# Performance work log

Measured on AMD Instinct MI355X. Metric: run time of the kernel, lower is better.

The kernel has to match this reference:

```python
import jax, jax.numpy as jnp
import numpy as np

N_NODES = 100000
N_EDGES = 3200000
FEAT = 16


def gcn_conv(x, src, dst, W, b):
    # PyG GCNConv: add self-loops, symmetric normalization deg^{-1/2}(A+I)deg^{-1/2},
    # then linear transform and scatter-add aggregation.
    n = x.shape[0]
    loop = jnp.arange(n, dtype=src.dtype)
    s = jnp.concatenate([src, loop])
    d = jnp.concatenate([dst, loop])
    deg = jax.ops.segment_sum(jnp.ones_like(d, dtype=x.dtype), d, num_segments=n)
    dinv = jnp.where(deg > 0, jax.lax.rsqrt(deg), 0.0)
    norm = dinv[s] * dinv[d]  # [E+N]
    h = x @ W  # [N, out]
    msg = h[s] * norm[:, None]  # gather + weight
    out = jax.ops.segment_sum(msg, d, num_segments=n)  # scatter-add
    return out + b


def setup_inputs() -> dict:
    key = jax.random.key(0)
    k1, k2, k3, k4 = jax.random.split(key, 4)
    scale = 1.0 / np.sqrt(FEAT)
    return {
        "x": jax.random.normal(k1, (N_NODES, FEAT), dtype=jnp.float32),
        "edge_index": jax.random.randint(k2, (2, N_EDGES), 0, N_NODES, dtype=jnp.int64) if jax.config.jax_enable_x64 else jax.random.randint(k2, (2, N_EDGES), 0, N_NODES, dtype=jnp.int32),
        "W1": jax.random.normal(k3, (FEAT, 16), dtype=jnp.float32) * scale,
        "b1": jnp.zeros((16,), dtype=jnp.float32),
        "W2": jax.random.normal(k4, (16, FEAT), dtype=jnp.float32) * scale,
        "b2": jnp.zeros((FEAT,), dtype=jnp.float32),
    }


def reference(x, edge_index, W1, b1, W2, b2):
    src, dst = edge_index[0], edge_index[1]
    h = gcn_conv(x, src, dst, W1, b1)
    h = jax.nn.relu(h)
    out = gcn_conv(h, src, dst, W2, b2)
    return out
```

## Files before the change

kernel.cpp:

```cpp
#include <hip/hip_runtime.h>

#define F 16
#define BSHIFT 8
#define NPB 256
#define NB 391
#define CH 4096


__global__ void hist_kernel(const int* __restrict__ dst, unsigned* __restrict__ bcount, int E) {
    __shared__ unsigned lc[NB];
    for (int i = threadIdx.x; i < NB; i += blockDim.x) lc[i] = 0;
    __syncthreads();
    int E4 = E >> 2;
    const int4* d4 = (const int4*)dst;
    int stride = gridDim.x * blockDim.x;
    for (int e = blockIdx.x * blockDim.x + threadIdx.x; e < E4; e += stride) {
        int4 v = d4[e];
        atomicAdd(&lc[((unsigned)v.x) >> BSHIFT], 1u);
        atomicAdd(&lc[((unsigned)v.y) >> BSHIFT], 1u);
        atomicAdd(&lc[((unsigned)v.z) >> BSHIFT], 1u);
        atomicAdd(&lc[((unsigned)v.w) >> BSHIFT], 1u);
    }
    for (int e = E4 * 4 + blockIdx.x * blockDim.x + threadIdx.x; e < E; e += stride)
        atomicAdd(&lc[((unsigned)dst[e]) >> BSHIFT], 1u);
    __syncthreads();
    for (int i = threadIdx.x; i < NB; i += blockDim.x) {
        unsigned c = lc[i];
        if (c) atomicAdd(&bcount[i], c);
    }
}

__global__ void scan_kernel(const unsigned* __restrict__ bcount, int* __restrict__ off,
                            unsigned* __restrict__ cursor, int E) {
    __shared__ unsigned s[2048];
    int t = threadIdx.x;
    unsigned c0 = (t < NB) ? bcount[t] : 0u;
    unsigned c1 = (t + 1024 < NB) ? bcount[t + 1024] : 0u;
    s[t] = c0; s[t + 1024] = c1;
    __syncthreads();
    for (int d = 1; d < 2048; d <<= 1) {
        unsigned a  = (t >= d) ? s[t - d] : 0u;
        unsigned bv = (t + 1024 >= d) ? s[t + 1024 - d] : 0u;
        __syncthreads();
        s[t] += a; s[t + 1024] += bv;
        __syncthreads();
    }
    if (t < NB)       { unsigned ex = s[t] - c0;       off[t] = ex;       cursor[t * 16] = ex; }
    if (t + 1024 < NB){ unsigned ex = s[t+1024] - c1;  off[t+1024] = ex;  cursor[(t+1024)*16] = ex; }
    if (t == 0) off[NB] = E;
}

__global__ void reorder_kernel(const int* __restrict__ src, const int* __restrict__ dst,
                               unsigned* __restrict__ cursor, unsigned* __restrict__ recs, int E) {
    __shared__ unsigned lsorted[CH];
    __shared__ unsigned short lbkt[CH];
    __shared__ unsigned lstart[NB + 1];
    __shared__ unsigned lcur[NB];
    __shared__ int ldelta[NB];
    int t = threadIdx.x, b = blockIdx.x;
    int e0 = b * CH;
    int cnt_e = E - e0; if (cnt_e > CH) cnt_e = CH;
    int i4 = cnt_e >> 2;
    const int4* dst4 = (const int4*)(dst + e0);
    const int4* src4 = (const int4*)(src + e0);

    for (int i = t; i < NB; i += 512) lcur[i] = 0;
    __syncthreads();
    for (int i = t; i < i4; i += 512) {
        int4 d = dst4[i];
        atomicAdd(&lcur[((unsigned)d.x) >> BSHIFT], 1u);
        atomicAdd(&lcur[((unsigned)d.y) >> BSHIFT], 1u);
        atomicAdd(&lcur[((unsigned)d.z) >> BSHIFT], 1u);
        atomicAdd(&lcur[((unsigned)d.w) >> BSHIFT], 1u);
    }
    for (int i = i4 * 4 + t; i < cnt_e; i += 512)
        atomicAdd(&lcur[((unsigned)dst[e0 + i]) >> BSHIFT], 1u);
    __syncthreads();
    if (t < 64) {
        unsigned run = 0;
        for (int c = 0; c < NB; c += 64) {
            int idx = c + t;
            unsigned v = (idx < NB) ? lcur[idx] : 0u;
            unsigned inc = v;
#pragma unroll
            for (int d = 1; d < 64; d <<= 1) {
                unsigned o = __shfl_up(inc, d, 64);
                if (t >= d) inc += o;
            }
            if (idx <= NB) lstart[idx] = run + inc - v;
            unsigned tot = __shfl(inc, 63, 64);
            if (t == 63 && idx < NB) lstart[idx + 1] = run + inc;
            run += tot;
        }
        if (t == 0) lstart[NB] = (unsigned)cnt_e;
    }
    __syncthreads();
    for (int i = t; i < NB; i += 512) {
        unsigned st = lstart[i];
        unsigned cnt = lstart[i + 1] - st;
        lcur[i] = st;
        if (cnt) {
            unsigned g = atomicAdd(&cursor[i * 16], cnt);
            ldelta[i] = (int)g - (int)st;
        }
    }
    __syncthreads();
    for (int i = t; i < i4; i += 512) {
        int4 d = dst4[i];
        int4 s = src4[i];
        unsigned dd, bk, pos;
        dd = (unsigned)d.x; bk = dd >> BSHIFT; pos = atomicAdd(&lcur[bk], 1u);
        lsorted[pos] = (unsigned)s.x | ((dd & (NPB - 1u)) << 17); lbkt[pos] = (unsigned short)bk;
        dd = (unsigned)d.y; bk = dd >> BSHIFT; pos = atomicAdd(&lcur[bk], 1u);
        lsorted[pos] = (unsigned)s.y | ((dd & (NPB - 1u)) << 17); lbkt[pos] = (unsigned short)bk;
        dd = (unsigned)d.z; bk = dd >> BSHIFT; pos = atomicAdd(&lcur[bk], 1u);
        lsorted[pos] = (unsigned)s.z | ((dd & (NPB - 1u)) << 17); lbkt[pos] = (unsigned short)bk;
        dd = (unsigned)d.w; bk = dd >> BSHIFT; pos = atomicAdd(&lcur[bk], 1u);
        lsorted[pos] = (unsigned)s.w | ((dd & (NPB - 1u)) << 17); lbkt[pos] = (unsigned short)bk;
    }
    for (int i = i4 * 4 + t; i < cnt_e; i += 512) {
        unsigned dd = (unsigned)dst[e0 + i];
        unsigned bk = dd >> BSHIFT;
        unsigned pos = atomicAdd(&lcur[bk], 1u);
        lsorted[pos] = (unsigned)src[e0 + i] | ((dd & (NPB - 1u)) << 17);
        lbkt[pos] = (unsigned short)bk;
    }
    __syncthreads();
    for (int i = t; i < cnt_e; i += 512) {
        unsigned bk = lbkt[i];
        recs[ldelta[bk] + i] = lsorted[i];
    }
}

__global__ void sort2_kernel(const unsigned* __restrict__ recs, const int* __restrict__ off,
                             unsigned* __restrict__ srcs, int* __restrict__ noff,
                             float* __restrict__ dinv, int n, int E) {
    __shared__ unsigned cnt[NPB];
    __shared__ unsigned curs[NPB];
    __shared__ unsigned wtot[4];
    int t = threadIdx.x, b = blockIdx.x;
    if (t < NPB) cnt[t] = 0;
    __syncthreads();
    int e0 = off[b], e1 = off[b + 1];
    for (int e = e0 + t; e < e1; e += 1024) atomicAdd(&cnt[recs[e] >> 17], 1u);
    __syncthreads();
    if (t < NPB) {
        unsigned c = cnt[t];
        unsigned inc = c;
        int lane = t & 63, w = t >> 6;
#pragma unroll
        for (int d = 1; d < 64; d <<= 1) {
            unsigned o = __shfl_up(inc, d, 64);
            if (lane >= d) inc += o;
        }
        if (lane == 63) wtot[w] = inc;
        __syncthreads();
        unsigned wbase = 0;
        for (int i = 0; i < w; ++i) wbase += wtot[i];
        unsigned ex = wbase + inc - c;
        curs[t] = (unsigned)e0 + ex;
        int node = b * NPB + t;
        if (node < n) {
            noff[node] = e0 + (int)ex;
            dinv[node] = rsqrtf((float)c + 1.0f);
        }
    } else {
        __syncthreads();
    }
    if (b == (int)gridDim.x - 1 && t == 0) noff[n] = E;
    __syncthreads();
    for (int e = e0 + t; e < e1; e += 1024) {
        unsigned rec = recs[e];
        unsigned pos = atomicAdd(&curs[rec >> 17], 1u);
        srcs[pos] = rec & 0x1FFFFu;
    }
}

__global__ void linear_kernel(const float* __restrict__ in, const float* __restrict__ dinv,
                              const float* __restrict__ W, float* __restrict__ out, int n) {
    __shared__ float Ws[F * F];
    __shared__ float As[64][F + 1];
    int t = threadIdx.x;
    Ws[t] = W[t];
    int g = t >> 2, c = t & 3;
    int node = blockIdx.x * 64 + g;
    float4 v = {0.f, 0.f, 0.f, 0.f};
    if (node < n) v = ((const float4*)in)[(size_t)node * 4 + c];
    As[g][c * 4 + 0] = v.x; As[g][c * 4 + 1] = v.y;
    As[g][c * 4 + 2] = v.z; As[g][c * 4 + 3] = v.w;
    __syncthreads();
    if (node < n) {
        float di = dinv[node];
        float4 o = {0.f, 0.f, 0.f, 0.f};
        int j = c * 4;
#pragma unroll
        for (int k = 0; k < F; ++k) {
            float ak = As[g][k];
            o.x += ak * Ws[k * F + j + 0];
            o.y += ak * Ws[k * F + j + 1];
            o.z += ak * Ws[k * F + j + 2];
            o.w += ak * Ws[k * F + j + 3];
        }
        o.x *= di; o.y *= di; o.z *= di; o.w *= di;
        ((float4*)out)[(size_t)node * 4 + c] = o;
    }
}

__global__ void agg_csr_kernel(const float* __restrict__ hin, const unsigned* __restrict__ srcs,
                               const int* __restrict__ noff, const float* __restrict__ dinv,
                               const float* __restrict__ Wn, const float* __restrict__ bias,
                               float* __restrict__ outp, int n, int mode) {
    __shared__ float a1[64][F + 1];
    __shared__ float Ws[F * F];
    int t = threadIdx.x;
    int g = t >> 2, c = t & 3;
    if (mode == 1) Ws[t] = Wn[t];
    int node = blockIdx.x * 64 + g;
    const float4* h4 = (const float4*)hin;
    float4 val = {0.f, 0.f, 0.f, 0.f};
    float di = 0.f;
    if (node < n) {
        di = dinv[node];
        int e0 = noff[node], e1 = noff[node + 1];
        float4 s0 = {0,0,0,0}, s1 = {0,0,0,0}, s2 = {0,0,0,0}, s3 = {0,0,0,0};
        int e = e0;
        for (; e + 4 <= e1; e += 4) {
            int ia = srcs[e], ib = srcs[e + 1], ic = srcs[e + 2], id = srcs[e + 3];
            float4 va = h4[(size_t)ia * 4 + c];
            float4 vb = h4[(size_t)ib * 4 + c];
            float4 vc = h4[(size_t)ic * 4 + c];
            float4 vd = h4[(size_t)id * 4 + c];
            s0.x += va.x; s0.y += va.y; s0.z += va.z; s0.w += va.w;
            s1.x += vb.x; s1.y += vb.y; s1.z += vb.z; s1.w += vb.w;
            s2.x += vc.x; s2.y += vc.y; s2.z += vc.z; s2.w += vc.w;
            s3.x += vd.x; s3.y += vd.y; s3.z += vd.z; s3.w += vd.w;
        }
        for (; e < e1; ++e) {
            float4 va = h4[(size_t)srcs[e] * 4 + c];
            s0.x += va.x; s0.y += va.y; s0.z += va.z; s0.w += va.w;
        }
        float4 self = h4[(size_t)node * 4 + c];
        float4 bi = ((const float4*)bias)[c];
        val.x = di * ((s0.x + s1.x) + (s2.x + s3.x) + self.x) + bi.x;
        val.y = di * ((s0.y + s1.y) + (s2.y + s3.y) + self.y) + bi.y;
        val.z = di * ((s0.z + s1.z) + (s2.z + s3.z) + self.z) + bi.z;
        val.w = di * ((s0.w + s1.w) + (s2.w + s3.w) + self.w) + bi.w;
        if (mode == 1) {
            val.x = fmaxf(val.x, 0.f); val.y = fmaxf(val.y, 0.f);
            val.z = fmaxf(val.z, 0.f); val.w = fmaxf(val.w, 0.f);
        }
    }
    if (mode == 1) {
        a1[g][c * 4 + 0] = val.x; a1[g][c * 4 + 1] = val.y;
        a1[g][c * 4 + 2] = val.z; a1[g][c * 4 + 3] = val.w;
        __syncthreads();
        if (node < n) {
            float4 o = {0.f, 0.f, 0.f, 0.f};
            int j = c * 4;
#pragma unroll
            for (int k = 0; k < F; ++k) {
                float ak = a1[g][k];
                o.x += ak * Ws[k * F + j + 0];
                o.y += ak * Ws[k * F + j + 1];
                o.z += ak * Ws[k * F + j + 2];
                o.w += ak * Ws[k * F + j + 3];
            }
            o.x *= di; o.y *= di; o.z *= di; o.w *= di;
            ((float4*)outp)[(size_t)node * 4 + c] = o;
        }
    } else {
        if (node < n) ((float4*)outp)[(size_t)node * 4 + c] = val;
    }
}


__global__ void deg_kernel(const int* __restrict__ dst, float* __restrict__ deg, int E) {
    int e = blockIdx.x * blockDim.x + threadIdx.x;
    if (e < E) atomicAdd(&deg[dst[e]], 1.0f);
}
__global__ void dinv_kernel(float* __restrict__ deg, int n) {
    int i = blockIdx.x * blockDim.x + threadIdx.x;
    if (i < n) deg[i] = rsqrtf(deg[i] + 1.0f);
}
__global__ void linear2_kernel(const float* __restrict__ in, const float* __restrict__ acc,
                               const float* __restrict__ dinv, const float* __restrict__ W,
                               const float* __restrict__ bias, float* __restrict__ out,
                               int n, int mode) {
    __shared__ float Ws[F * F];
    __shared__ float As[16][F + 1];
    int t = threadIdx.x;
    Ws[t] = W[t];
    int nb = t >> 4, j = t & 15;
    int i = blockIdx.x * 16 + nb;
    float di = 0.f, v = 0.f;
    if (i < n) {
        di = dinv[i]; v = in[i * F + j];
        if (mode) { v = di * (acc[i * F + j] + v) + bias[j]; v = fmaxf(v, 0.f); }
    }
    As[nb][j] = v;
    __syncthreads();
    if (i < n) {
        float s = 0.f;
#pragma unroll
        for (int k = 0; k < F; ++k) s += As[nb][k] * Ws[k * F + j];
        out[i * F + j] = s * di;
    }
}
__global__ void scatter_kernel(const int* __restrict__ src, const int* __restrict__ dst,
                               const float* __restrict__ h, float* __restrict__ acc, int E) {
    int t = blockIdx.x * blockDim.x + threadIdx.x;
    int e = t >> 4, j = t & 15;
    if (e < E) atomicAdd(&acc[dst[e] * F + j], h[src[e] * F + j]);
}
__global__ void out_kernel(const float* __restrict__ acc, const float* __restrict__ h,
                           const float* __restrict__ dinv, const float* __restrict__ bias,
                           float* __restrict__ out, int n) {
    int t = blockIdx.x * blockDim.x + threadIdx.x;
    if (t < n * F) {
        int i = t >> 4, j = t & 15;
        out[t] = dinv[i] * (acc[t] + h[t]) + bias[j];
    }
}


extern "C" void kernel_launch(void* const* d_in, const int* in_sizes, int n_in,
                              void* d_out, int out_size, void* d_ws, size_t ws_size,
                              hipStream_t stream) {
    const float* x  = (const float*)d_in[0];
    const int*   ei = (const int*)d_in[1];
    const float* W1 = (const float*)d_in[2];
    const float* b1 = (const float*)d_in[3];
    const float* W2 = (const float*)d_in[4];
    const float* b2 = (const float*)d_in[5];
    float* outp = (float*)d_out;

    const int N = in_sizes[0] / F;
    const int E = in_sizes[1] / 2;
    const int* src = ei;
    const int* dst = ei + E;

    const int nb_rt = (N + NPB - 1) >> BSHIFT;
    size_t need = sizeof(float) * ((size_t)N * 33 + (N + 1)
                                   + 2 * (size_t)E + NB + (NB + 1) + 16 * NB);

    if (nb_rt == NB && ws_size >= need) {
        float* dinv = (float*)d_ws;
        float* hA = dinv + N;
        float* hB = hA + (size_t)F * N;
        unsigned* recs = (unsigned*)(hB + (size_t)F * N);
        unsigned* srcs = recs + E;
        int* noff = (int*)(srcs + E);
        unsigned* bcount = (unsigned*)(noff + N + 1);
        int* off = (int*)(bcount + NB);
        unsigned* cursor = (unsigned*)(off + NB + 1);

        hipMemsetAsync(bcount, 0, NB * sizeof(unsigned), stream);
        hist_kernel<<<512, 256, 0, stream>>>(dst, bcount, E);
        scan_kernel<<<1, 1024, 0, stream>>>(bcount, off, cursor, E);
        reorder_kernel<<<(E + CH - 1) / CH, 512, 0, stream>>>(src, dst, cursor, recs, E);
        sort2_kernel<<<NB, 1024, 0, stream>>>(recs, off, srcs, noff, dinv, N, E);
        linear_kernel<<<(N + 63) / 64, 256, 0, stream>>>(x, dinv, W1, hA, N);
        agg_csr_kernel<<<(N + 63) / 64, 256, 0, stream>>>(hA, srcs, noff, dinv, W2, b1, hB, N, 1);
        agg_csr_kernel<<<(N + 63) / 64, 256, 0, stream>>>(hB, srcs, noff, dinv, nullptr, b2, outp, N, 2);
    } else {
        float* dinv = (float*)d_ws;
        float* h = dinv + N;
        float* acc = h + (size_t)F * N;
        hipMemsetAsync(dinv, 0, (size_t)N * sizeof(float), stream);
        hipMemsetAsync(acc, 0, (size_t)F * N * sizeof(float), stream);
        deg_kernel<<<(E + 255) / 256, 256, 0, stream>>>(dst, dinv, E);
        dinv_kernel<<<(N + 255) / 256, 256, 0, stream>>>(dinv, N);
        linear2_kernel<<<(N + 15) / 16, 256, 0, stream>>>(x, nullptr, dinv, W1, nullptr, h, N, 0);
        scatter_kernel<<<((size_t)E * F + 255) / 256, 256, 0, stream>>>(src, dst, h, acc, E);
        linear2_kernel<<<(N + 15) / 16, 256, 0, stream>>>(h, acc, dinv, W2, b1, h, N, 1);
        hipMemsetAsync(acc, 0, (size_t)F * N * sizeof(float), stream);
        scatter_kernel<<<((size_t)E * F + 255) / 256, 256, 0, stream>>>(src, dst, h, acc, E);
        out_kernel<<<((size_t)N * F + 255) / 256, 256, 0, stream>>>(acc, h, dinv, b2, outp, N);
    }
}
```

Measured before the change: 242.6 us.

## Split feature columns into halves so gather tables fit cache better

The hidden features are stored as two 8-column halves, and each aggregation pass runs separately per half (four aggregation launches instead of two). Each half table is 3.2 MB instead of 6.4 MB, so random gathers are more likely to hit in L2 or the infinity cache. Edge index loads also become nontemporal. The cost is that the CSR index array is read twice per layer, along with extra launches and an intermediate buffer.

```diff
diff --git a/kernel.cpp b/kernel.cpp
--- a/kernel.cpp
+++ b/kernel.cpp
@@ -176,8 +176,9 @@
     }
 }
 
-__global__ void linear_kernel(const float* __restrict__ in, const float* __restrict__ dinv,
-                              const float* __restrict__ W, float* __restrict__ out, int n) {
+__global__ void linear_split_kernel(const float* __restrict__ in, const float* __restrict__ dinv,
+                                    const float* __restrict__ W,
+                                    float4* __restrict__ o0, float4* __restrict__ o1, int n) {
     __shared__ float Ws[F * F];
     __shared__ float As[64][F + 1];
     int t = threadIdx.x;
@@ -202,74 +203,96 @@
             o.w += ak * Ws[k * F + j + 3];
         }
         o.x *= di; o.y *= di; o.z *= di; o.w *= di;
-        ((float4*)out)[(size_t)node * 4 + c] = o;
-    }
-}
-
-__global__ void agg_csr_kernel(const float* __restrict__ hin, const unsigned* __restrict__ srcs,
-                               const int* __restrict__ noff, const float* __restrict__ dinv,
-                               const float* __restrict__ Wn, const float* __restrict__ bias,
-                               float* __restrict__ outp, int n, int mode) {
-    __shared__ float a1[64][F + 1];
+        if (c < 2) o0[(size_t)node * 2 + c] = o;
+        else       o1[(size_t)node * 2 + (c - 2)] = o;
+    }
+}
+
+__global__ void agg_half_kernel(const float4* __restrict__ hin, const unsigned* __restrict__ srcs,
+                                const int* __restrict__ noff, const float* __restrict__ dinv,
+                                const float* __restrict__ Wn, const float* __restrict__ bias8,
+                                const float4* __restrict__ alo_in,
+                                float4* __restrict__ o0, float4* __restrict__ o1,
+                                int n, int mode) {
+    __shared__ float al[128][F + 1];
     __shared__ float Ws[F * F];
     int t = threadIdx.x;
-    int g = t >> 2, c = t & 3;
+    int g = t >> 1, c = t & 1;
     if (mode == 1) Ws[t] = Wn[t];
-    int node = blockIdx.x * 64 + g;
-    const float4* h4 = (const float4*)hin;
+    int node = blockIdx.x * 128 + g;
+    float di = 0.f;
     float4 val = {0.f, 0.f, 0.f, 0.f};
-    float di = 0.f;
     if (node < n) {
         di = dinv[node];
         int e0 = noff[node], e1 = noff[node + 1];
         float4 s0 = {0,0,0,0}, s1 = {0,0,0,0}, s2 = {0,0,0,0}, s3 = {0,0,0,0};
         int e = e0;
         for (; e + 4 <= e1; e += 4) {
-            int ia = srcs[e], ib = srcs[e + 1], ic = srcs[e + 2], id = srcs[e + 3];
-            float4 va = h4[(size_t)ia * 4 + c];
-            float4 vb = h4[(size_t)ib * 4 + c];
-            float4 vc = h4[(size_t)ic * 4 + c];
-            float4 vd = h4[(size_t)id * 4 + c];
+            unsigned ia = __builtin_nontemporal_load(srcs + e);
+            unsigned ib = __builtin_nontemporal_load(srcs + e + 1);
+            unsigned ic = __builtin_nontemporal_load(srcs + e + 2);
+            unsigned id = __builtin_nontemporal_load(srcs + e + 3);
+            float4 va = hin[(size_t)ia * 2 + c];
+            float4 vb = hin[(size_t)ib * 2 + c];
+            float4 vc = hin[(size_t)ic * 2 + c];
+            float4 vd = hin[(size_t)id * 2 + c];
             s0.x += va.x; s0.y += va.y; s0.z += va.z; s0.w += va.w;
             s1.x += vb.x; s1.y += vb.y; s1.z += vb.z; s1.w += vb.w;
             s2.x += vc.x; s2.y += vc.y; s2.z += vc.z; s2.w += vc.w;
             s3.x += vd.x; s3.y += vd.y; s3.z += vd.z; s3.w += vd.w;
         }
         for (; e < e1; ++e) {
-            float4 va = h4[(size_t)srcs[e] * 4 + c];
+            unsigned ia = __builtin_nontemporal_load(srcs + e);
+            float4 va = hin[(size_t)ia * 2 + c];
             s0.x += va.x; s0.y += va.y; s0.z += va.z; s0.w += va.w;
         }
-        float4 self = h4[(size_t)node * 4 + c];
-        float4 bi = ((const float4*)bias)[c];
+        float4 self = hin[(size_t)node * 2 + c];
+        float4 bi = ((const float4*)bias8)[c];
         val.x = di * ((s0.x + s1.x) + (s2.x + s3.x) + self.x) + bi.x;
         val.y = di * ((s0.y + s1.y) + (s2.y + s3.y) + self.y) + bi.y;
         val.z = di * ((s0.z + s1.z) + (s2.z + s3.z) + self.z) + bi.z;
         val.w = di * ((s0.w + s1.w) + (s2.w + s3.w) + self.w) + bi.w;
-        if (mode == 1) {
+        if (mode <= 1) {
             val.x = fmaxf(val.x, 0.f); val.y = fmaxf(val.y, 0.f);
             val.z = fmaxf(val.z, 0.f); val.w = fmaxf(val.w, 0.f);
         }
     }
-    if (mode == 1) {
-        a1[g][c * 4 + 0] = val.x; a1[g][c * 4 + 1] = val.y;
-        a1[g][c * 4 + 2] = val.z; a1[g][c * 4 + 3] = val.w;
+    if (mode == 0) {
+        if (node < n) o0[(size_t)node * 2 + c] = val;
+    } else if (mode == 1) {
+        if (node < n) {
+            float4 av = alo_in[(size_t)node * 2 + c];
+            al[g][c * 4 + 0] = av.x; al[g][c * 4 + 1] = av.y;
+            al[g][c * 4 + 2] = av.z; al[g][c * 4 + 3] = av.w;
+            al[g][8 + c * 4 + 0] = val.x; al[g][8 + c * 4 + 1] = val.y;
+            al[g][8 + c * 4 + 2] = val.z; al[g][8 + c * 4 + 3] = val.w;
+        }
         __syncthreads();
         if (node < n) {
-            float4 o = {0.f, 0.f, 0.f, 0.f};
-            int j = c * 4;
+            int j0 = c * 8;
+            float4 oa = {0,0,0,0}, ob = {0,0,0,0};
 #pragma unroll
             for (int k = 0; k < F; ++k) {
-                float ak = a1[g][k];
-                o.x += ak * Ws[k * F + j + 0];
-                o.y += ak * Ws[k * F + j + 1];
-                o.z += ak * Ws[k * F + j + 2];
-                o.w += ak * Ws[k * F + j + 3];
+                float ak = al[g][k];
+                oa.x += ak * Ws[k * F + j0 + 0];
+                oa.y += ak * Ws[k * F + j0 + 1];
+                oa.z += ak * Ws[k * F + j0 + 2];
+                oa.w += ak * Ws[k * F + j0 + 3];
+                ob.x += ak * Ws[k * F + j0 + 4];
+                ob.y += ak * Ws[k * F + j0 + 5];
+                ob.z += ak * Ws[k * F + j0 + 6];
+                ob.w += ak * Ws[k * F + j0 + 7];
             }
-            o.x *= di; o.y *= di; o.z *= di; o.w *= di;
-            ((float4*)outp)[(size_t)node * 4 + c] = o;
-        }
+            oa.x *= di; oa.y *= di; oa.z *= di; oa.w *= di;
+            ob.x *= di; ob.y *= di; ob.z *= di; ob.w *= di;
+            float4* dstp = (c == 0) ? o0 : o1;
+            dstp[(size_t)node * 2 + 0] = oa;
+            dstp[(size_t)node * 2 + 1] = ob;
+        }
+    } else if (mode == 2) {
+        if (node < n) o0[(size_t)node * 4 + c] = val;
     } else {
-        if (node < n) ((float4*)outp)[(size_t)node * 4 + c] = val;
+        if (node < n) o0[(size_t)node * 4 + 2 + c] = val;
     }
 }
 
@@ -345,23 +368,37 @@
 
     if (nb_rt == NB && ws_size >= need) {
         float* dinv = (float*)d_ws;
-        float* hA = dinv + N;
-        float* hB = hA + (size_t)F * N;
-        unsigned* recs = (unsigned*)(hB + (size_t)F * N);
+        float* h0 = dinv + N;
+        float* h1 = h0 + (size_t)8 * N;
+        float* alo = h1 + (size_t)8 * N;
+        float* g1 = alo + (size_t)8 * N;
+        unsigned* recs = (unsigned*)(g1 + (size_t)8 * N);
         unsigned* srcs = recs + E;
         int* noff = (int*)(srcs + E);
         unsigned* bcount = (unsigned*)(noff + N + 1);
         int* off = (int*)(bcount + NB);
         unsigned* cursor = (unsigned*)(off + NB + 1);
+        float* g0 = h0;
 
         hipMemsetAsync(bcount, 0, NB * sizeof(unsigned), stream);
         hist_kernel<<<512, 256, 0, stream>>>(dst, bcount, E);
         scan_kernel<<<1, 1024, 0, stream>>>(bcount, off, cursor, E);
         reorder_kernel<<<(E + CH - 1) / CH, 512, 0, stream>>>(src, dst, cursor, recs, E);
         sort2_kernel<<<NB, 1024, 0, stream>>>(recs, off, srcs, noff, dinv, N, E);
-        linear_kernel<<<(N + 63) / 64, 256, 0, stream>>>(x, dinv, W1, hA, N);
-        agg_csr_kernel<<<(N + 63) / 64, 256, 0, stream>>>(hA, srcs, noff, dinv, W2, b1, hB, N, 1);
-        agg_csr_kernel<<<(N + 63) / 64, 256, 0, stream>>>(hB, srcs, noff, dinv, nullptr, b2, outp, N, 2);
+        linear_split_kernel<<<(N + 63) / 64, 256, 0, stream>>>(x, dinv, W1, (float4*)h0, (float4*)h1, N);
+        int agrid = (N + 127) / 128;
+        agg_half_kernel<<<agrid, 256, 0, stream>>>((const float4*)h0, srcs, noff, dinv,
+                                                   nullptr, b1, nullptr,
+                                                   (float4*)alo, nullptr, N, 0);
+        agg_half_kernel<<<agrid, 256, 0, stream>>>((const float4*)h1, srcs, noff, dinv,
+                                                   W2, b1 + 8, (const float4*)alo,
+                                                   (float4*)g0, (float4*)g1, N, 1);
+        agg_half_kernel<<<agrid, 256, 0, stream>>>((const float4*)g0, srcs, noff, dinv,
+                                                   nullptr, b2, nullptr,
+                                                   (float4*)outp, nullptr, N, 2);
+        agg_half_kernel<<<agrid, 256, 0, stream>>>((const float4*)g1, srcs, noff, dinv,
+                                                   nullptr, b2 + 8, nullptr,
+                                                   (float4*)outp, nullptr, N, 3);
     } else {
         float* dinv = (float*)d_ws;
         float* h = dinv + N;
```

Measured after the change: 324.1 us. 1.34x slower.

## Replace histogram and scan passes with fixed-capacity bucket slots in the CSR build

Applied to the files above, without the earlier changes.

Drops the global histogram and scan kernels. Each coarse dst bucket now gets a fixed slot of BCAP records, with cursors seeded by a tiny init kernel. reorder_kernel reads dst once, keeps per-edge bucket, rank and low bits in registers, and scatters from there instead of re-reading dst. sort2_kernel sorts each bucket in shared memory and writes srcs coalesced, using per-node noff/nend ranges, and hB reuses the recs buffer. It saves launches and global passes, but nothing checks bucket overflow, so heavily skewed degree distributions would write out of bounds.

```diff
diff --git a/kernel.cpp b/kernel.cpp
--- a/kernel.cpp
+++ b/kernel.cpp
@@ -5,144 +5,106 @@
 #define NPB 256
 #define NB 391
 #define CH 4096
-
-
-__global__ void hist_kernel(const int* __restrict__ dst, unsigned* __restrict__ bcount, int E) {
-    __shared__ unsigned lc[NB];
-    for (int i = threadIdx.x; i < NB; i += blockDim.x) lc[i] = 0;
-    __syncthreads();
-    int E4 = E >> 2;
-    const int4* d4 = (const int4*)dst;
-    int stride = gridDim.x * blockDim.x;
-    for (int e = blockIdx.x * blockDim.x + threadIdx.x; e < E4; e += stride) {
-        int4 v = d4[e];
-        atomicAdd(&lc[((unsigned)v.x) >> BSHIFT], 1u);
-        atomicAdd(&lc[((unsigned)v.y) >> BSHIFT], 1u);
-        atomicAdd(&lc[((unsigned)v.z) >> BSHIFT], 1u);
-        atomicAdd(&lc[((unsigned)v.w) >> BSHIFT], 1u);
-    }
-    for (int e = E4 * 4 + blockIdx.x * blockDim.x + threadIdx.x; e < E; e += stride)
-        atomicAdd(&lc[((unsigned)dst[e]) >> BSHIFT], 1u);
-    __syncthreads();
-    for (int i = threadIdx.x; i < NB; i += blockDim.x) {
-        unsigned c = lc[i];
-        if (c) atomicAdd(&bcount[i], c);
-    }
-}
-
-__global__ void scan_kernel(const unsigned* __restrict__ bcount, int* __restrict__ off,
-                            unsigned* __restrict__ cursor, int E) {
-    __shared__ unsigned s[2048];
-    int t = threadIdx.x;
-    unsigned c0 = (t < NB) ? bcount[t] : 0u;
-    unsigned c1 = (t + 1024 < NB) ? bcount[t + 1024] : 0u;
-    s[t] = c0; s[t + 1024] = c1;
-    __syncthreads();
-    for (int d = 1; d < 2048; d <<= 1) {
-        unsigned a  = (t >= d) ? s[t - d] : 0u;
-        unsigned bv = (t + 1024 >= d) ? s[t + 1024 - d] : 0u;
-        __syncthreads();
-        s[t] += a; s[t + 1024] += bv;
-        __syncthreads();
-    }
-    if (t < NB)       { unsigned ex = s[t] - c0;       off[t] = ex;       cursor[t * 16] = ex; }
-    if (t + 1024 < NB){ unsigned ex = s[t+1024] - c1;  off[t+1024] = ex;  cursor[(t+1024)*16] = ex; }
-    if (t == 0) off[NB] = E;
-}
-
-__global__ void reorder_kernel(const int* __restrict__ src, const int* __restrict__ dst,
-                               unsigned* __restrict__ cursor, unsigned* __restrict__ recs, int E) {
+#define BCAP 9216
+
+
+__global__ void init_cursor_kernel(unsigned* __restrict__ cursor) {
+    int i = threadIdx.x;
+    if (i < NB) cursor[i * 16] = (unsigned)(i * BCAP);
+}
+
+__global__ __launch_bounds__(512) void
+reorder_kernel(const int* __restrict__ src, const int* __restrict__ dst,
+               unsigned* __restrict__ cursor, unsigned* __restrict__ recs, int E) {
     __shared__ unsigned lsorted[CH];
     __shared__ unsigned short lbkt[CH];
+    __shared__ unsigned cnt[NB];
     __shared__ unsigned lstart[NB + 1];
-    __shared__ unsigned lcur[NB];
-    __shared__ int ldelta[NB];
     int t = threadIdx.x, b = blockIdx.x;
     int e0 = b * CH;
     int cnt_e = E - e0; if (cnt_e > CH) cnt_e = CH;
-    int i4 = cnt_e >> 2;
-    const int4* dst4 = (const int4*)(dst + e0);
-    const int4* src4 = (const int4*)(src + e0);
-
-    for (int i = t; i < NB; i += 512) lcur[i] = 0;
-    __syncthreads();
-    for (int i = t; i < i4; i += 512) {
-        int4 d = dst4[i];
-        atomicAdd(&lcur[((unsigned)d.x) >> BSHIFT], 1u);
-        atomicAdd(&lcur[((unsigned)d.y) >> BSHIFT], 1u);
-        atomicAdd(&lcur[((unsigned)d.z) >> BSHIFT], 1u);
-        atomicAdd(&lcur[((unsigned)d.w) >> BSHIFT], 1u);
-    }
-    for (int i = i4 * 4 + t; i < cnt_e; i += 512)
-        atomicAdd(&lcur[((unsigned)dst[e0 + i]) >> BSHIFT], 1u);
+
+    for (int i = t; i < NB; i += 512) cnt[i] = 0;
+    __syncthreads();
+    unsigned pk[8];
+#pragma unroll
+    for (int j = 0; j < 8; ++j) {
+        int i = t + j * 512;
+        pk[j] = 0xFFFFFFFFu;
+        if (i < cnt_e) {
+            unsigned d = (unsigned)dst[e0 + i];
+            unsigned bk = d >> BSHIFT;
+            unsigned r = atomicAdd(&cnt[bk], 1u);
+            pk[j] = bk | ((d & 255u) << 9) | (r << 17);
+        }
+    }
     __syncthreads();
     if (t < 64) {
         unsigned run = 0;
         for (int c = 0; c < NB; c += 64) {
             int idx = c + t;
-            unsigned v = (idx < NB) ? lcur[idx] : 0u;
+            unsigned v = (idx < NB) ? cnt[idx] : 0u;
             unsigned inc = v;
 #pragma unroll
             for (int d = 1; d < 64; d <<= 1) {
                 unsigned o = __shfl_up(inc, d, 64);
                 if (t >= d) inc += o;
             }
-            if (idx <= NB) lstart[idx] = run + inc - v;
-            unsigned tot = __shfl(inc, 63, 64);
-            if (t == 63 && idx < NB) lstart[idx + 1] = run + inc;
-            run += tot;
+            if (idx < NB) lstart[idx] = run + inc - v;
+            run += __shfl(inc, 63, 64);
         }
         if (t == 0) lstart[NB] = (unsigned)cnt_e;
     }
     __syncthreads();
     for (int i = t; i < NB; i += 512) {
-        unsigned st = lstart[i];
-        unsigned cnt = lstart[i + 1] - st;
-        lcur[i] = st;
-        if (cnt) {
-            unsigned g = atomicAdd(&cursor[i * 16], cnt);
-            ldelta[i] = (int)g - (int)st;
-        }
-    }
-    __syncthreads();
-    for (int i = t; i < i4; i += 512) {
-        int4 d = dst4[i];
-        int4 s = src4[i];
-        unsigned dd, bk, pos;
-        dd = (unsigned)d.x; bk = dd >> BSHIFT; pos = atomicAdd(&lcur[bk], 1u);
-        lsorted[pos] = (unsigned)s.x | ((dd & (NPB - 1u)) << 17); lbkt[pos] = (unsigned short)bk;
-        dd = (unsigned)d.y; bk = dd >> BSHIFT; pos = atomicAdd(&lcur[bk], 1u);
-        lsorted[pos] = (unsigned)s.y | ((dd & (NPB - 1u)) << 17); lbkt[pos] = (unsigned short)bk;
-        dd = (unsigned)d.z; bk = dd >> BSHIFT; pos = atomicAdd(&lcur[bk], 1u);
-        lsorted[pos] = (unsigned)s.z | ((dd & (NPB - 1u)) << 17); lbkt[pos] = (unsigned short)bk;
-        dd = (unsigned)d.w; bk = dd >> BSHIFT; pos = atomicAdd(&lcur[bk], 1u);
-        lsorted[pos] = (unsigned)s.w | ((dd & (NPB - 1u)) << 17); lbkt[pos] = (unsigned short)bk;
-    }
-    for (int i = i4 * 4 + t; i < cnt_e; i += 512) {
-        unsigned dd = (unsigned)dst[e0 + i];
-        unsigned bk = dd >> BSHIFT;
-        unsigned pos = atomicAdd(&lcur[bk], 1u);
-        lsorted[pos] = (unsigned)src[e0 + i] | ((dd & (NPB - 1u)) << 17);
-        lbkt[pos] = (unsigned short)bk;
+        unsigned c = cnt[i];
+        if (c) cnt[i] = atomicAdd(&cursor[i * 16], c);
+    }
+    __syncthreads();
+#pragma unroll
+    for (int j = 0; j < 8; ++j) {
+        int i = t + j * 512;
+        if (i < cnt_e) {
+            unsigned p = pk[j];
+            unsigned bk = p & 0x1FFu;
+            unsigned low = (p >> 9) & 255u;
+            unsigned r = p >> 17;
+            unsigned pos = lstart[bk] + r;
+            lsorted[pos] = (unsigned)src[e0 + i] | (low << 17);
+            lbkt[pos] = (unsigned short)bk;
+        }
     }
     __syncthreads();
     for (int i = t; i < cnt_e; i += 512) {
         unsigned bk = lbkt[i];
-        recs[ldelta[bk] + i] = lsorted[i];
-    }
-}
-
-__global__ void sort2_kernel(const unsigned* __restrict__ recs, const int* __restrict__ off,
-                             unsigned* __restrict__ srcs, int* __restrict__ noff,
-                             float* __restrict__ dinv, int n, int E) {
+        recs[cnt[bk] + ((unsigned)i - lstart[bk])] = lsorted[i];
+    }
+}
+
+__global__ __launch_bounds__(1024) void
+sort2_kernel(const unsigned* __restrict__ recs, const unsigned* __restrict__ cursor,
+             unsigned* __restrict__ srcs, int* __restrict__ noff, int* __restrict__ nend,
+             float* __restrict__ dinv, int n) {
+    __shared__ unsigned lsort[BCAP];
     __shared__ unsigned cnt[NPB];
-    __shared__ unsigned curs[NPB];
+    __shared__ unsigned ex[NPB];
     __shared__ unsigned wtot[4];
     int t = threadIdx.x, b = blockIdx.x;
+    int e0 = b * BCAP;
+    int used = (int)(cursor[b * 16] - (unsigned)e0);
     if (t < NPB) cnt[t] = 0;
     __syncthreads();
-    int e0 = off[b], e1 = off[b + 1];
-    for (int e = e0 + t; e < e1; e += 1024) atomicAdd(&cnt[recs[e] >> 17], 1u);
+    unsigned pk[9];
+#pragma unroll
+    for (int j = 0; j < 9; ++j) {
+        int i = t + j * 1024;
+        pk[j] = 0xFFFFFFFFu;
+        if (i < used) {
+            unsigned node = recs[e0 + i] >> 17;
+            unsigned r = atomicAdd(&cnt[node], 1u);
+            pk[j] = node | (r << 8);
+        }
+    }
     __syncthreads();
     if (t < NPB) {
         unsigned c = cnt[t];
@@ -157,23 +119,28 @@
         __syncthreads();
         unsigned wbase = 0;
         for (int i = 0; i < w; ++i) wbase += wtot[i];
-        unsigned ex = wbase + inc - c;
-        curs[t] = (unsigned)e0 + ex;
+        unsigned e = wbase + inc - c;
+        ex[t] = e;
         int node = b * NPB + t;
         if (node < n) {
-            noff[node] = e0 + (int)ex;
+            noff[node] = e0 + (int)e;
+            nend[node] = e0 + (int)(e + c);
             dinv[node] = rsqrtf((float)c + 1.0f);
         }
     } else {
         __syncthreads();
     }
-    if (b == (int)gridDim.x - 1 && t == 0) noff[n] = E;
-    __syncthreads();
-    for (int e = e0 + t; e < e1; e += 1024) {
-        unsigned rec = recs[e];
-        unsigned pos = atomicAdd(&curs[rec >> 17], 1u);
-        srcs[pos] = rec & 0x1FFFFu;
-    }
+    __syncthreads();
+#pragma unroll
+    for (int j = 0; j < 9; ++j) {
+        int i = t + j * 1024;
+        if (i < used) {
+            unsigned p = pk[j];
+            lsort[ex[p & 255u] + (p >> 8)] = recs[e0 + i] & 0x1FFFFu;
+        }
+    }
+    __syncthreads();
+    for (int i = t; i < used; i += 1024) srcs[e0 + i] = lsort[i];
 }
 
 __global__ void linear_kernel(const float* __restrict__ in, const float* __restrict__ dinv,
@@ -207,7 +174,8 @@
 }
 
 __global__ void agg_csr_kernel(const float* __restrict__ hin, const unsigned* __restrict__ srcs,
-                               const int* __restrict__ noff, const float* __restrict__ dinv,
+                               const int* __restrict__ noff, const int* __restrict__ nend,
+                               const float* __restrict__ dinv,
                                const float* __restrict__ Wn, const float* __restrict__ bias,
                                float* __restrict__ outp, int n, int mode) {
     __shared__ float a1[64][F + 1];
@@ -221,7 +189,7 @@
     float di = 0.f;
     if (node < n) {
         di = dinv[node];
-        int e0 = noff[node], e1 = noff[node + 1];
+        int e0 = noff[node], e1 = nend[node];
         float4 s0 = {0,0,0,0}, s1 = {0,0,0,0}, s2 = {0,0,0,0}, s3 = {0,0,0,0};
         int e = e0;
         for (; e + 4 <= e1; e += 4) {
@@ -340,28 +308,25 @@
     const int* dst = ei + E;
 
     const int nb_rt = (N + NPB - 1) >> BSHIFT;
-    size_t need = sizeof(float) * ((size_t)N * 33 + (N + 1)
-                                   + 2 * (size_t)E + NB + (NB + 1) + 16 * NB);
-
-    if (nb_rt == NB && ws_size >= need) {
+    const size_t RC = (size_t)NB * BCAP;
+    size_t need = sizeof(unsigned) * ((size_t)N * 19 + 2 * RC + 16 * NB);
+
+    if (nb_rt == NB && E <= CH * 65535 && ws_size >= need) {
         float* dinv = (float*)d_ws;
         float* hA = dinv + N;
-        float* hB = hA + (size_t)F * N;
-        unsigned* recs = (unsigned*)(hB + (size_t)F * N);
-        unsigned* srcs = recs + E;
-        int* noff = (int*)(srcs + E);
-        unsigned* bcount = (unsigned*)(noff + N + 1);
-        int* off = (int*)(bcount + NB);
-        unsigned* cursor = (unsigned*)(off + NB + 1);
-
-        hipMemsetAsync(bcount, 0, NB * sizeof(unsigned), stream);
-        hist_kernel<<<512, 256, 0, stream>>>(dst, bcount, E);
-        scan_kernel<<<1, 1024, 0, stream>>>(bcount, off, cursor, E);
+        unsigned* recs = (unsigned*)(hA + (size_t)F * N);
+        float* hB = (float*)recs;
+        unsigned* srcs = recs + RC;
+        int* noff = (int*)(srcs + RC);
+        int* nend = noff + N;
+        unsigned* cursor = (unsigned*)(nend + N);
+
+        init_cursor_kernel<<<1, 512, 0, stream>>>(cursor);
         reorder_kernel<<<(E + CH - 1) / CH, 512, 0, stream>>>(src, dst, cursor, recs, E);
-        sort2_kernel<<<NB, 1024, 0, stream>>>(recs, off, srcs, noff, dinv, N, E);
+        sort2_kernel<<<NB, 1024, 0, stream>>>(recs, cursor, srcs, noff, nend, dinv, N);
         linear_kernel<<<(N + 63) / 64, 256, 0, stream>>>(x, dinv, W1, hA, N);
-        agg_csr_kernel<<<(N + 63) / 64, 256, 0, stream>>>(hA, srcs, noff, dinv, W2, b1, hB, N, 1);
-        agg_csr_kernel<<<(N + 63) / 64, 256, 0, stream>>>(hB, srcs, noff, dinv, nullptr, b2, outp, N, 2);
+        agg_csr_kernel<<<(N + 63) / 64, 256, 0, stream>>>(hA, srcs, noff, nend, dinv, W2, b1, hB, N, 1);
+        agg_csr_kernel<<<(N + 63) / 64, 256, 0, stream>>>(hB, srcs, noff, nend, dinv, nullptr, b2, outp, N, 2);
     } else {
         float* dinv = (float*)d_ws;
         float* h = dinv + N;
```

Result: faster. 214.1 us (-11.8%).
